# Kernel tuning notes

Measured on AMD Instinct MI355X. Metric: run time of the kernel, lower is better.

The kernel has to match this reference:

```python
import jax, jax.numpy as jnp
import numpy as np

N_NODES = 50000
N_EDGES = 800000
NFEAT, NHID, NCLASS = 256, 128, 32
MAX_DEG = 48  # safe upper bound on in-degree: mean 16 (+1 self loop), Poisson tail << 48


def _median_conv(x, src, dst, W, b, max_deg=MAX_DEG):
    """MedianConv: h = x @ W; remove self loops; add one self loop per node;
    per-destination median aggregation (lower median, like torch.median); + bias."""
    N, F = x.shape[0], W.shape[1]
    h = x @ W  # [N, F]
    # torch: remove_self_loops then add_self_loops -> effective edges are all
    # non-self edges plus exactly one self loop per node. Route original self
    # loops into a trash segment (index N) to keep shapes static.
    dst_eff = jnp.where(src == dst, N, dst)
    ar = jnp.arange(N)
    src_all = jnp.concatenate([src, ar])          # [E+N]
    dst_all = jnp.concatenate([dst_eff, ar])      # [E+N]
    E = src_all.shape[0]
    order = jnp.argsort(dst_all)                  # group edges by destination
    d_s = dst_all[order]
    msg = h[src_all[order]]                       # [E+N, F] gathered messages
    deg = jax.ops.segment_sum(jnp.ones(E, jnp.int32), d_s, num_segments=N + 1)
    offsets = jnp.cumsum(deg) - deg               # start of each segment
    pos = jnp.arange(E) - offsets[d_s]            # slot within segment
    # dense batch padded with +inf so padding sorts to the end
    dense = jnp.full((N + 1, max_deg, F), jnp.inf, h.dtype)
    dense = dense.at[d_s, pos].set(msg)
    dense = jnp.sort(dense, axis=1)               # per-feature sort within segment
    med_idx = (deg[:N] - 1) // 2                  # lower median (torch.median)
    out = jnp.take_along_axis(dense[:N], med_idx[:, None, None], axis=1)[:, 0, :]
    return out + b


def setup_inputs() -> dict:
    key = jax.random.key(0)
    k1, k2, k3, k4, k5, k6 = jax.random.split(key, 6)
    features = jax.random.normal(k1, (N_NODES, NFEAT), dtype=jnp.float32)
    edge_index = jax.random.randint(k2, (2, N_EDGES), 0, N_NODES, dtype=jnp.int64)
    # Linear weights stored as [in, out] (transpose of torch layout)
    W1 = jax.random.normal(k3, (NFEAT, NHID), dtype=jnp.float32) * 0.05
    b1 = jnp.zeros((NHID,), dtype=jnp.float32)
    W2 = jax.random.normal(k4, (NHID, NCLASS), dtype=jnp.float32) * 0.05
    b2 = jnp.zeros((NCLASS,), dtype=jnp.float32)
    return {"features": features, "edge_index": edge_index,
            "W1": W1, "b1": b1, "W2": W2, "b2": b2}


def reference(features, edge_index, W1, b1, W2, b2):
    src, dst = edge_index[0], edge_index[1]
    # dropout is identity in eval mode
    x = _median_conv(features, src, dst, W1, b1)
    x = jax.nn.relu(x)
    x = _median_conv(x, src, dst, W2, b2)
    return jax.nn.log_softmax(x, axis=1)
```

## Files before the change

kernel.cpp:

```cpp
#include <hip/hip_runtime.h>
#include <hip/hip_bf16.h>
#include <math.h>

#define N_NODES 50000
#define N_EDGES 800000
#define NFEAT 256
#define NHID 128
#define NCLASS 32
#define STRIDE 48
#define G1B 782

#define INFF __builtin_inff()

typedef unsigned short ushort_t;
typedef unsigned int uint_t;
typedef __bf16 bf16x8 __attribute__((ext_vector_type(8)));
typedef float f32x4 __attribute__((ext_vector_type(4)));
typedef unsigned short u16x2 __attribute__((ext_vector_type(2)));

__device__ __forceinline__ float bf2f(ushort_t u) {
  union { unsigned int i; float f; } c;
  c.i = ((unsigned int)u) << 16;
  return c.f;
}
__device__ __forceinline__ ushort_t f2bf(float f) {
  unsigned int x = __float_as_uint(f);
  unsigned int r = (x + 0x7fff + ((x >> 16) & 1)) >> 16;
  return (ushort_t)r;
}
__device__ __forceinline__ ushort_t bf2sort(ushort_t b) {
  return b ^ ((b & 0x8000) ? 0xFFFFu : 0x8000u);
}
__device__ __forceinline__ ushort_t sort2bf(ushort_t s) {
  return s ^ ((s & 0x8000) ? 0x8000u : 0xFFFFu);
}


__global__ __launch_bounds__(256) void pre_k(const float* __restrict__ X,
                                             const float* __restrict__ W,
                                             ushort_t* __restrict__ H1,
                                             const int* __restrict__ src,
                                             const int* __restrict__ dst,
                                             int* __restrict__ cur,
                                             ushort_t* __restrict__ adjw) {
  __shared__ ushort_t As[64][40];
  __shared__ ushort_t Bs[128][40];
  int bid = blockIdx.x;
  int tid = threadIdx.x;

  if (bid >= G1B) {
    int i = (bid - G1B) * 256 + tid;
    if (i < N_EDGES) {
      int s = src[i], d = dst[i];
      if (s != d) {
        int p = atomicAdd(&cur[d], 1);
        if (p < STRIDE - 1) adjw[d * STRIDE + 1 + p] = (ushort_t)s;
      }
    } else {
      int v = i - N_EDGES;
      if (v < N_NODES) adjw[v * STRIDE] = (ushort_t)v;
    }
    return;
  }

  int rb = bid * 64;
  int lane = tid & 63, wid = tid >> 6;
  int wm = wid >> 1, wn = wid & 1;
  int lrow = lane & 15, lk = (lane >> 4) * 8;
  int arow = tid >> 2, akq = (tid & 3) * 8;
  int bn = tid & 127, bkh = tid >> 7;

  f32x4 acc[2][4];
#pragma unroll
  for (int m = 0; m < 2; ++m)
#pragma unroll
    for (int n = 0; n < 4; ++n) acc[m][n] = (f32x4){0.f, 0.f, 0.f, 0.f};

  for (int kc = 0; kc < NFEAT; kc += 32) {
    {
      int grow = rb + arow;
      bf16x8 p;
      if (grow < N_NODES) {
        const float* gp = X + (size_t)grow * NFEAT + kc + akq;
        float4 v0 = *reinterpret_cast<const float4*>(gp);
        float4 v1 = *reinterpret_cast<const float4*>(gp + 4);
        p[0] = (__bf16)v0.x; p[1] = (__bf16)v0.y; p[2] = (__bf16)v0.z; p[3] = (__bf16)v0.w;
        p[4] = (__bf16)v1.x; p[5] = (__bf16)v1.y; p[6] = (__bf16)v1.z; p[7] = (__bf16)v1.w;
      } else {
        p = (bf16x8)(__bf16)0.f;
      }
      *reinterpret_cast<bf16x8*>(&As[arow][akq]) = p;
    }
    {
      const float* gp = W + (size_t)(kc + bkh * 16) * NHID + bn;
      bf16x8 p0, p1;
#pragma unroll
      for (int j = 0; j < 8; ++j) p0[j] = (__bf16)gp[(size_t)j * NHID];
#pragma unroll
      for (int j = 0; j < 8; ++j) p1[j] = (__bf16)gp[(size_t)(8 + j) * NHID];
      *reinterpret_cast<bf16x8*>(&Bs[bn][bkh * 16]) = p0;
      *reinterpret_cast<bf16x8*>(&Bs[bn][bkh * 16 + 8]) = p1;
    }
    __syncthreads();
    bf16x8 af[2], bfr[4];
#pragma unroll
    for (int m = 0; m < 2; ++m)
      af[m] = *reinterpret_cast<const bf16x8*>(&As[wm * 32 + m * 16 + lrow][lk]);
#pragma unroll
    for (int n = 0; n < 4; ++n)
      bfr[n] = *reinterpret_cast<const bf16x8*>(&Bs[wn * 64 + n * 16 + lrow][lk]);
#pragma unroll
    for (int m = 0; m < 2; ++m)
#pragma unroll
      for (int n = 0; n < 4; ++n)
        acc[m][n] = __builtin_amdgcn_mfma_f32_16x16x32_bf16(af[m], bfr[n], acc[m][n], 0, 0, 0);
    __syncthreads();
  }
#pragma unroll
  for (int m = 0; m < 2; ++m) {
    int row0 = rb + wm * 32 + m * 16 + (lane >> 4) * 4;
#pragma unroll
    for (int n = 0; n < 4; ++n) {
      int col = wn * 64 + n * 16 + lrow;
#pragma unroll
      for (int j = 0; j < 4; ++j) {
        int r = row0 + j;
        if (r < N_NODES) H1[(size_t)r * NHID + col] = bf2sort(f2bf(acc[m][n][j]));
      }
    }
  }
}


__global__ __launch_bounds__(256) void gemm2_k(const uint_t* __restrict__ X1u,
                                               const float* __restrict__ W,
                                               ushort_t* __restrict__ H2s) {
  __shared__ ushort_t As[128][136];
  __shared__ ushort_t Bs[32][136];
  int tid = threadIdx.x;
  int rb = blockIdx.x * 128;
  int lane = tid & 63, wid = tid >> 6;
  int lrow = lane & 15, lk = (lane >> 4) * 8;

#pragma unroll
  for (int j = 0; j < 8; ++j) {
    int f = tid + j * 256;
    int row = f >> 4;
    int q = f & 15;
    int grow = rb + row;
    uint4 v = make_uint4(0, 0, 0, 0);
    if (grow < N_NODES)
      v = *reinterpret_cast<const uint4*>(X1u + (size_t)grow * 64 + q * 4);
    *reinterpret_cast<uint4*>(&As[row][q * 8]) = v;
  }
  {
    int bn = tid & 31, bq = tid >> 5;
    const float* gp = W + (size_t)(bq * 16) * NCLASS + bn;
    bf16x8 p0, p1;
#pragma unroll
    for (int j = 0; j < 8; ++j) p0[j] = (__bf16)gp[(size_t)j * NCLASS];
#pragma unroll
    for (int j = 0; j < 8; ++j) p1[j] = (__bf16)gp[(size_t)(8 + j) * NCLASS];
    *reinterpret_cast<bf16x8*>(&Bs[bn][bq * 16]) = p0;
    *reinterpret_cast<bf16x8*>(&Bs[bn][bq * 16 + 8]) = p1;
  }
  __syncthreads();

  f32x4 acc[2][2];
#pragma unroll
  for (int m = 0; m < 2; ++m)
#pragma unroll
    for (int n = 0; n < 2; ++n) acc[m][n] = (f32x4){0.f, 0.f, 0.f, 0.f};

#pragma unroll
  for (int ks = 0; ks < 4; ++ks) {
    bf16x8 af[2], bfr[2];
#pragma unroll
    for (int m = 0; m < 2; ++m)
      af[m] = *reinterpret_cast<const bf16x8*>(&As[wid * 32 + m * 16 + lrow][ks * 32 + lk]);
#pragma unroll
    for (int n = 0; n < 2; ++n)
      bfr[n] = *reinterpret_cast<const bf16x8*>(&Bs[n * 16 + lrow][ks * 32 + lk]);
#pragma unroll
    for (int m = 0; m < 2; ++m)
#pragma unroll
      for (int n = 0; n < 2; ++n)
        acc[m][n] = __builtin_amdgcn_mfma_f32_16x16x32_bf16(af[m], bfr[n], acc[m][n], 0, 0, 0);
  }
#pragma unroll
  for (int m = 0; m < 2; ++m) {
    int row0 = rb + wid * 32 + m * 16 + (lane >> 4) * 4;
#pragma unroll
    for (int n = 0; n < 2; ++n) {
      int col = n * 16 + lrow;
#pragma unroll
      for (int j = 0; j < 4; ++j) {
        int r = row0 + j;
        if (r < N_NODES) H2s[(size_t)r * NCLASS + col] = bf2sort(f2bf(acc[m][n][j]));
      }
    }
  }
}


template <int NP>
__device__ __forceinline__ void pk_sort(u16x2 (&a)[NP]) {
#pragma unroll
  for (int p = 1; p < NP; p <<= 1) {
#pragma unroll
    for (int q = p; q >= 1; q >>= 1) {
#pragma unroll
      for (int j = q % p; j + q < NP; j += 2 * q) {
#pragma unroll
        for (int i = 0; i < q; ++i) {
          int lo = i + j, hi = i + j + q;
          if (hi < NP && (lo / (2 * p)) == (hi / (2 * p))) {
            u16x2 x = a[lo], y = a[hi];
            a[lo] = __builtin_elementwise_min(x, y);
            a[hi] = __builtin_elementwise_max(x, y);
          }
        }
      }
    }
  }
}


template <int KP>
__device__ __forceinline__ uint_t med1_path(const uint_t* __restrict__ H1p, int sreg,
                                            int k, int m, int t) {
  u16x2 a[KP];
#pragma unroll
  for (int e = 0; e < KP; ++e) {
    int s = __builtin_amdgcn_readlane(sreg, e);
    uint_t u = H1p[(size_t)s * 64 + t];
    uint_t pu = (e < k) ? u : 0xFFFFFFFFu;
    union { uint_t u; u16x2 v; } c;
    c.u = pu;
    a[e] = c.v;
  }
  pk_sort<KP>(a);
  u16x2 med = a[0];
#pragma unroll
  for (int i = 1; i <= (KP - 1) / 2; ++i)
    if (i == m) med = a[i];
  union { u16x2 v; uint_t u; } r;
  r.v = med;
  return r.u;
}

__global__ __launch_bounds__(256, 8) void med1_k(const ushort_t* __restrict__ H1,
                                                 const int* __restrict__ cur,
                                                 const ushort_t* __restrict__ adjw,
                                                 const float* __restrict__ b1,
                                                 uint_t* __restrict__ X1u) {
  int v = blockIdx.x * 4 + (threadIdx.x >> 6);
  int t = threadIdx.x & 63;
  int k = cur[v] + 1;
  if (k > STRIDE) k = STRIDE;
  int sreg = adjw[v * STRIDE + ((t < k) ? t : 0)];
  int m = (k - 1) >> 1;
  const uint_t* H1p = reinterpret_cast<const uint_t*>(H1);
  uint_t mu;
  if (k <= 16)      mu = med1_path<16>(H1p, sreg, k, m, t);
  else if (k <= 32) mu = med1_path<32>(H1p, sreg, k, m, t);
  else              mu = med1_path<48>(H1p, sreg, k, m, t);
  ushort_t s0 = (ushort_t)(mu & 0xFFFF), s1 = (ushort_t)(mu >> 16);
  float2 bb = *reinterpret_cast<const float2*>(b1 + 2 * t);
  float f0 = fmaxf(bf2f(sort2bf(s0)) + bb.x, 0.f);
  float f1 = fmaxf(bf2f(sort2bf(s1)) + bb.y, 0.f);
  X1u[(size_t)v * 64 + t] = (uint_t)f2bf(f0) | ((uint_t)f2bf(f1) << 16);
}


template <int KP>
__device__ __forceinline__ uint_t med2_path(const uint_t* __restrict__ H2p,
                                            int s0, int s1, int s2,
                                            int k, int m, int g, int l) {
  u16x2 a[KP];
#pragma unroll
  for (int e = 0; e < KP; ++e) {
    int sr = (e < 16) ? s0 : ((e < 32) ? s1 : s2);
    int srcid = __shfl(sr, g * 16 + (e & 15), 64);
    uint_t u = H2p[(size_t)srcid * 16 + l];
    uint_t pu = (e < k) ? u : 0xFFFFFFFFu;
    union { uint_t u; u16x2 v; } c;
    c.u = pu;
    a[e] = c.v;
  }
  pk_sort<KP>(a);
  u16x2 med = a[0];
#pragma unroll
  for (int i = 1; i <= (KP - 1) / 2; ++i)
    if (i == m) med = a[i];
  union { u16x2 v; uint_t u; } r;
  r.v = med;
  return r.u;
}

__global__ __launch_bounds__(256, 8) void med2_k(const ushort_t* __restrict__ H2,
                                                 const int* __restrict__ cur,
                                                 const ushort_t* __restrict__ adjw,
                                                 const float* __restrict__ b2,
                                                 float* __restrict__ OUT) {
  int w = threadIdx.x >> 6;
  int t = threadIdx.x & 63;
  int l = t & 15, g = t >> 4;
  int vh = (blockIdx.x * 4 + w) * 4 + g;
  int k = cur[vh] + 1;
  if (k > STRIDE) k = STRIDE;
  int m = (k - 1) >> 1;
  int base = vh * STRIDE;
  int s0 = adjw[base + ((l < k) ? l : 0)];
  int s1 = adjw[base + ((16 + l < k) ? 16 + l : 0)];
  int s2 = adjw[base + ((32 + l < k) ? 32 + l : 0)];
  int kmax = max(k, __shfl_xor(k, 16, 64));
  kmax = max(kmax, __shfl_xor(kmax, 32, 64));
  const uint_t* H2p = reinterpret_cast<const uint_t*>(H2);
  uint_t mu;
  if (kmax <= 16)      mu = med2_path<16>(H2p, s0, s1, s2, k, m, g, l);
  else if (kmax <= 32) mu = med2_path<32>(H2p, s0, s1, s2, k, m, g, l);
  else                 mu = med2_path<48>(H2p, s0, s1, s2, k, m, g, l);
  ushort_t u0 = (ushort_t)(mu & 0xFFFF), u1 = (ushort_t)(mu >> 16);
  float2 bb = *reinterpret_cast<const float2*>(b2 + 2 * l);
  float f0 = bf2f(sort2bf(u0)) + bb.x;
  float f1 = bf2f(sort2bf(u1)) + bb.y;
  float mx = fmaxf(f0, f1);
#pragma unroll
  for (int s = 8; s; s >>= 1) mx = fmaxf(mx, __shfl_xor(mx, s, 16));
  float sum = expf(f0 - mx) + expf(f1 - mx);
#pragma unroll
  for (int s = 8; s; s >>= 1) sum += __shfl_xor(sum, s, 16);
  float lg = logf(sum);
  float2 res = make_float2(f0 - mx - lg, f1 - mx - lg);
  *reinterpret_cast<float2*>(&OUT[(size_t)vh * NCLASS + 2 * l]) = res;
}


extern "C" void kernel_launch(void* const* d_in, const int* in_sizes, int n_in,
                              void* d_out, int out_size, void* d_ws, size_t ws_size,
                              hipStream_t stream) {
  const float* X = (const float*)d_in[0];
  const int* src = (const int*)d_in[1];
  const int* dst = src + N_EDGES;
  const float* W1 = (const float*)d_in[2];
  const float* b1 = (const float*)d_in[3];
  const float* W2 = (const float*)d_in[4];
  const float* b2 = (const float*)d_in[5];
  float* OUT = (float*)d_out;

  char* w = (char*)d_ws;
  size_t o = 0;
  auto take = [&](size_t bytes) {
    void* p = w + o;
    o += (bytes + 255) & ~(size_t)255;
    return p;
  };
  int* cur = (int*)take(N_NODES * sizeof(int));
  ushort_t* adjw = (ushort_t*)take((size_t)N_NODES * STRIDE * sizeof(ushort_t));
  ushort_t* h1 = (ushort_t*)take((size_t)N_NODES * NHID * sizeof(ushort_t));
  uint_t* x1 = (uint_t*)take((size_t)N_NODES * 64 * sizeof(uint_t));
  ushort_t* h2 = (ushort_t*)take((size_t)N_NODES * NCLASS * sizeof(ushort_t));
  (void)ws_size;

  hipMemsetAsync(cur, 0, N_NODES * sizeof(int), stream);
  int scatter_blocks = (N_EDGES + N_NODES + 255) / 256;
  pre_k<<<G1B + scatter_blocks, 256, 0, stream>>>(X, W1, h1, src, dst, cur, adjw);
  med1_k<<<N_NODES / 4, 256, 0, stream>>>(h1, cur, adjw, b1, x1);
  gemm2_k<<<(N_NODES + 127) / 128, 256, 0, stream>>>(x1, W2, h2);
  med2_k<<<N_NODES / 16, 256, 0, stream>>>(h2, cur, adjw, b2, OUT);
}
```

Baseline: 117.0 us.

## Partition edge scatter by XCD with work-stealing chunk queues

The edge scatter is now a persistent, chunked work-stealing sweep. Each block reads its XCD id from a hardware register and first handles the chunks whose destination nodes fall in its XCD's node range, then cycles through the other ranges. The goal is to keep the atomics and adjacency writes for a node slice local to one XCD's L2 and to let GEMM blocks join the scatter once their tile is done. The cost is that every block rereads every edge chunk's dst for each of the 8 ranges, which multiplies dst read traffic, and the two syncthreads per chunk add overhead.

```diff
diff --git a/kernel.cpp b/kernel.cpp
--- a/kernel.cpp
+++ b/kernel.cpp
@@ -9,6 +9,12 @@
 #define NCLASS 32
 #define STRIDE 48
 #define G1B 782
+#define SCAT_BLOCKS 1024
+#define CHUNK 2048
+#define TOT_ITEMS (N_EDGES + N_NODES)
+#define NCH ((TOT_ITEMS + CHUNK - 1) / CHUNK)
+#define NODES_PER_XCD (N_NODES / 8)
+#define HWREG_XCC_ID ((3 << 11) | 20)
 
 #define INFF __builtin_inff()
 
@@ -33,6 +39,45 @@
 }
 __device__ __forceinline__ ushort_t sort2bf(ushort_t s) {
   return s ^ ((s & 0x8000) ? 0x8000u : 0xFFFFu);
+}
+
+__device__ __forceinline__ void scatter_sweep(const int* __restrict__ src,
+                                              const int* __restrict__ dst,
+                                              int* __restrict__ cur,
+                                              ushort_t* __restrict__ adjw,
+                                              int* shc_p, int tid) {
+  int xcd = __builtin_amdgcn_s_getreg(HWREG_XCC_ID) & 7;
+  int* qcnt = cur + N_NODES;
+  for (int q = 0; q < 8; ++q) {
+    int qx = (xcd + q) & 7;
+    int lo = qx * NODES_PER_XCD;
+    int hi = lo + NODES_PER_XCD;
+    for (;;) {
+      if (tid == 0) *shc_p = atomicAdd(&qcnt[qx], 1);
+      __syncthreads();
+      int c = *shc_p;
+      __syncthreads();
+      if (c >= NCH) break;
+      int base = c * CHUNK + tid;
+#pragma unroll
+      for (int j = 0; j < CHUNK / 256; ++j) {
+        int i = base + j * 256;
+        if (i < N_EDGES) {
+          int d = dst[i];
+          if (d >= lo && d < hi) {
+            int s = src[i];
+            if (s != d) {
+              int p = atomicAdd(&cur[d], 1);
+              if (p < STRIDE - 1) adjw[d * STRIDE + 1 + p] = (ushort_t)s;
+            }
+          }
+        } else {
+          int v = i - N_EDGES;
+          if (v < N_NODES && v >= lo && v < hi) adjw[v * STRIDE] = (ushort_t)v;
+        }
+      }
+    }
+  }
 }
 
 
@@ -45,21 +90,12 @@
                                              ushort_t* __restrict__ adjw) {
   __shared__ ushort_t As[64][40];
   __shared__ ushort_t Bs[128][40];
+  __shared__ int shc;
   int bid = blockIdx.x;
   int tid = threadIdx.x;
 
   if (bid >= G1B) {
-    int i = (bid - G1B) * 256 + tid;
-    if (i < N_EDGES) {
-      int s = src[i], d = dst[i];
-      if (s != d) {
-        int p = atomicAdd(&cur[d], 1);
-        if (p < STRIDE - 1) adjw[d * STRIDE + 1 + p] = (ushort_t)s;
-      }
-    } else {
-      int v = i - N_EDGES;
-      if (v < N_NODES) adjw[v * STRIDE] = (ushort_t)v;
-    }
+    scatter_sweep(src, dst, cur, adjw, &shc, tid);
     return;
   }
 
@@ -129,6 +165,8 @@
       }
     }
   }
+  __syncthreads();
+  scatter_sweep(src, dst, cur, adjw, &shc, tid);
 }
 
 
@@ -356,16 +394,15 @@
     o += (bytes + 255) & ~(size_t)255;
     return p;
   };
-  int* cur = (int*)take(N_NODES * sizeof(int));
+  int* cur = (int*)take((N_NODES + 8) * sizeof(int));
   ushort_t* adjw = (ushort_t*)take((size_t)N_NODES * STRIDE * sizeof(ushort_t));
   ushort_t* h1 = (ushort_t*)take((size_t)N_NODES * NHID * sizeof(ushort_t));
   uint_t* x1 = (uint_t*)take((size_t)N_NODES * 64 * sizeof(uint_t));
   ushort_t* h2 = (ushort_t*)take((size_t)N_NODES * NCLASS * sizeof(ushort_t));
   (void)ws_size;
 
-  hipMemsetAsync(cur, 0, N_NODES * sizeof(int), stream);
-  int scatter_blocks = (N_EDGES + N_NODES + 255) / 256;
-  pre_k<<<G1B + scatter_blocks, 256, 0, stream>>>(X, W1, h1, src, dst, cur, adjw);
+  hipMemsetAsync(cur, 0, (N_NODES + 8) * sizeof(int), stream);
+  pre_k<<<G1B + SCAT_BLOCKS, 256, 0, stream>>>(X, W1, h1, src, dst, cur, adjw);
   med1_k<<<N_NODES / 4, 256, 0, stream>>>(h1, cur, adjw, b1, x1);
   gemm2_k<<<(N_NODES + 127) / 128, 256, 0, stream>>>(x1, W2, h2);
   med2_k<<<N_NODES / 16, 256, 0, stream>>>(h2, cur, adjw, b2, OUT);
```

Result: slower. 298.6 us (+155.2%).

## Partition edge scatter by destination node range across scatter blocks

Applied to the files above, without the earlier changes.

The scatter part of pre_k now runs on a fixed set of 1024 blocks arranged as 8 destination ranges by 128 edge slices. Each block scans one slice of 6250 edges and handles only edges whose destination lies in its range. The aim is to keep the atomics and adjacency writes of concurrent blocks confined to a narrower address region, for better cache locality and less atomic contention. The cost is that every edge's dst is read 8 times, and each block loops over 25 strided iterations instead of handling one edge per thread.

```diff
diff --git a/kernel.cpp b/kernel.cpp
--- a/kernel.cpp
+++ b/kernel.cpp
@@ -9,6 +9,9 @@
 #define NCLASS 32
 #define STRIDE 48
 #define G1B 782
+#define SCAT_BLOCKS 1024
+#define NODES_PER_RANGE (N_NODES / 8)
+#define EDGES_PER_SLICE (N_EDGES / 128)
 
 #define INFF __builtin_inff()
 
@@ -49,16 +52,31 @@
   int tid = threadIdx.x;
 
   if (bid >= G1B) {
-    int i = (bid - G1B) * 256 + tid;
-    if (i < N_EDGES) {
-      int s = src[i], d = dst[i];
-      if (s != d) {
-        int p = atomicAdd(&cur[d], 1);
-        if (p < STRIDE - 1) adjw[d * STRIDE + 1 + p] = (ushort_t)s;
-      }
-    } else {
-      int v = i - N_EDGES;
-      if (v < N_NODES) adjw[v * STRIDE] = (ushort_t)v;
+    int sb = bid - G1B;
+    int r = bid & 7;
+    int q = sb >> 3;
+    int lo = r * NODES_PER_RANGE, hi = lo + NODES_PER_RANGE;
+    if (tid < 49) {
+      int nl = q * 49 + tid;
+      if (nl < NODES_PER_RANGE) {
+        int v = lo + nl;
+        adjw[v * STRIDE] = (ushort_t)v;
+      }
+    }
+    int ebase = q * EDGES_PER_SLICE;
+    for (int j = 0; j < 25; ++j) {
+      int li = j * 256 + tid;
+      if (li < EDGES_PER_SLICE) {
+        int i = ebase + li;
+        int d = dst[i];
+        if (d >= lo && d < hi) {
+          int s = src[i];
+          if (s != d) {
+            int p = atomicAdd(&cur[d], 1);
+            if (p < STRIDE - 1) adjw[d * STRIDE + 1 + p] = (ushort_t)s;
+          }
+        }
+      }
     }
     return;
   }
@@ -364,8 +382,7 @@
   (void)ws_size;
 
   hipMemsetAsync(cur, 0, N_NODES * sizeof(int), stream);
-  int scatter_blocks = (N_EDGES + N_NODES + 255) / 256;
-  pre_k<<<G1B + scatter_blocks, 256, 0, stream>>>(X, W1, h1, src, dst, cur, adjw);
+  pre_k<<<G1B + SCAT_BLOCKS, 256, 0, stream>>>(X, W1, h1, src, dst, cur, adjw);
   med1_k<<<N_NODES / 4, 256, 0, stream>>>(h1, cur, adjw, b1, x1);
   gemm2_k<<<(N_NODES + 127) / 128, 256, 0, stream>>>(x1, W2, h2);
   med2_k<<<N_NODES / 16, 256, 0, stream>>>(h2, cur, adjw, b2, OUT);
```

Measured after the change: 125.5 us. +7.3%, slower.
